# Kernel tuning notes

Hardware: AMD Instinct MI355X
Metric: run time of the kernel (lower is better)

Reference implementation:

```python
import jax, jax.numpy as jnp
import numpy as np

F, R, H = 64, 8, 128  # feature_dim, response_dim, hidden_dim
EPS = 0.1


def _mk_linear(key, fan_in, fan_out):
    kw, kb = jax.random.split(key)
    lim = 1.0 / np.sqrt(fan_in)
    W = jax.random.uniform(kw, (fan_in, fan_out), jnp.float32, -lim, lim)
    b = jax.random.uniform(kb, (fan_out,), jnp.float32, -lim, lim)
    return W, b


def setup_inputs() -> dict:
    key = jax.random.key(0)
    ks = jax.random.split(key, 8)
    n, m = 1024, 1024
    X = jax.random.normal(ks[0], (n, F), jnp.float32)
    Y = jax.random.normal(ks[1], (n, R), jnp.float32)
    U = jax.random.normal(ks[2], (m, R), jnp.float32)
    W0, b0 = _mk_linear(ks[3], F + R, H)
    W1, b1 = _mk_linear(ks[4], H, H)
    W2, b2 = _mk_linear(ks[5], H, H)
    Wout, bout = _mk_linear(ks[6], H, 1)
    return {"X": X, "Y": Y, "U": U, "W0": W0, "b0": b0, "W1": W1,
            "b1": b1, "W2": W2, "b2": b2, "Wout": Wout, "bout": bout}


def _potential(X, U, W0, b0, W1, b1, W2, b2, Wout, bout):
    # X: [n, m, F], U: [n, m, R]  -> phi: [n, m]
    z = jnp.concatenate([X, U], axis=-1)
    h = jax.nn.softplus(z @ W0 + b0)
    h = jax.nn.softplus(h @ W1 + b1)
    h = jax.nn.softplus(h @ W2 + b2)
    return (h @ Wout + bout)[..., 0]


def reference(X, Y, U, W0, b0, W1, b1, W2, b2, Wout, bout):
    n = X.shape[0]
    m = U.shape[0]
    # expand to the pairwise [n, m, .] grid (broadcast views, no copy until MLP)
    Xe = jnp.broadcast_to(X[:, None, :], (n, m, F))
    Ue = jnp.broadcast_to(U[None, :, :], (n, m, R))
    phi = _potential(Xe, Ue, W0, b0, W1, b1, W2, b2, Wout, bout)  # [n, m]
    cost = Y @ U.T                                                # [n, m]
    slack = cost - phi
    # epsilon * (logsumexp(slack/eps) - log m) == stable max-shifted form in torch source
    lme = jax.scipy.special.logsumexp(slack / EPS, axis=-1, keepdims=True)
    lme = lme - jnp.log(jnp.asarray(m, slack.dtype))
    psi = EPS * lme                                               # [n, 1]
    return psi
```

## Files before the change

### kernel.cpp

```cpp
#include <hip/hip_runtime.h>
#include <math.h>


typedef __attribute__((ext_vector_type(8))) short short8;
typedef __attribute__((ext_vector_type(4))) float f32x4;

__device__ __forceinline__ float softplus_f(float x) {
    float ax = fabsf(x);
    float t = __logf(1.0f + __expf(-ax));
    return fmaxf(x, 0.0f) + t;
}

__device__ __forceinline__ unsigned short f2bf(float x) {
    unsigned int u = __float_as_uint(x);
    u = (u + 0x7FFFu + ((u >> 16) & 1u)) >> 16;
    return (unsigned short)u;
}

__device__ __forceinline__ float bf2f(unsigned short b) {
    return __uint_as_float(((unsigned int)b) << 16);
}

__global__ __launch_bounds__(128) void prep_kernel(
    const float* __restrict__ X, const float* __restrict__ U,
    const float* __restrict__ W0, const float* __restrict__ b0,
    const float* __restrict__ W1, const float* __restrict__ W2,
    float* __restrict__ A, float* __restrict__ Bu,
    unsigned short* __restrict__ w1t, unsigned short* __restrict__ w2t)
{
    const int b = blockIdx.x, t = threadIdx.x;
    if (b < 1024) {
        const float* xr = X + b * 64;
        float s = 0.f;
        #pragma unroll 8
        for (int f = 0; f < 64; ++f) s += xr[f] * W0[f * 128 + t];
        A[b * 128 + t] = s;
    } else if (b < 2048) {
        const int j = b - 1024;
        const float* ur = U + j * 8;
        float s = b0[t];
        #pragma unroll
        for (int r = 0; r < 8; ++r) s += ur[r] * W0[(64 + r) * 128 + t];
        Bu[j * 128 + t] = s;
    } else if (b < 2176) {
        const int n = b - 2048;
        w1t[n * 128 + t] = f2bf(W1[t * 128 + n]);
    } else {
        const int n = b - 2176;
        w2t[n * 128 + t] = f2bf(W2[t * 128 + n]);
    }
}

__global__ __launch_bounds__(256, 2) void main_kernel(
    const float* __restrict__ A, const float* __restrict__ Bu,
    const unsigned short* __restrict__ w1t, const unsigned short* __restrict__ w2t,
    const float* __restrict__ Y, const float* __restrict__ U,
    const float* __restrict__ b1, const float* __restrict__ b2,
    const float* __restrict__ Wout, const float* __restrict__ bout,
    float* __restrict__ part)
{
    __shared__ __align__(16) unsigned short Ha[64][136];
    __shared__ __align__(16) unsigned short Hb[64][136];
    __shared__ __align__(16) float A_lds[16][128];
    __shared__ __align__(16) float U_lds[64][8];
    __shared__ __align__(16) float Y_lds[16][8];
    __shared__ float slk[64];

    const int tid  = threadIdx.x;
    const int lane = tid & 63;
    const int w    = tid >> 6;
    const int ib   = blockIdx.x >> 4;
    const int jb   = blockIdx.x & 15;
    const int i0   = ib * 16;
    const int j0   = jb * 64;
    const int p    = tid >> 2;
    const int q    = tid & 3;

    {
        const float4* src = (const float4*)(A + i0 * 128);
        float4* dst = (float4*)(&A_lds[0][0]);
        dst[tid] = src[tid];
        dst[tid + 256] = src[tid + 256];
        if (tid < 128) ((float4*)U_lds)[tid] = ((const float4*)(U + j0 * 8))[tid];
        else if (tid < 160) ((float4*)Y_lds)[tid - 128] = ((const float4*)(Y + i0 * 8))[tid - 128];
    }

    float bu_reg[32];
    {
        const float4* src = (const float4*)(Bu + (j0 + p) * 128 + q * 32);
        #pragma unroll
        for (int v = 0; v < 8; ++v) {
            float4 f = src[v];
            bu_reg[v * 4 + 0] = f.x; bu_reg[v * 4 + 1] = f.y;
            bu_reg[v * 4 + 2] = f.z; bu_reg[v * 4 + 3] = f.w;
        }
    }

    short8 wf[2][2][4];
    {
        const int col = lane & 15;
        const int kk  = (lane >> 4) * 8;
        #pragma unroll
        for (int nt = 0; nt < 2; ++nt)
            #pragma unroll
            for (int ks = 0; ks < 4; ++ks) {
                wf[0][nt][ks] = *(const short8*)(w1t + (w * 32 + nt * 16 + col) * 128 + ks * 32 + kk);
                wf[1][nt][ks] = *(const short8*)(w2t + (w * 32 + nt * 16 + col) * 128 + ks * 32 + kk);
            }
    }
    float rb1[2], rb2[2];
    rb1[0] = b1[w * 32 + (lane & 15)];      rb1[1] = b1[w * 32 + 16 + (lane & 15)];
    rb2[0] = b2[w * 32 + (lane & 15)];      rb2[1] = b2[w * 32 + 16 + (lane & 15)];
    const float bo = bout[0];

    __syncthreads();

    for (int rd = 0; rd < 16; ++rd) {
        {
            const float* ar = &A_lds[rd][q * 32];
            unsigned short hv[32];
            #pragma unroll
            for (int e = 0; e < 32; ++e)
                hv[e] = f2bf(softplus_f(ar[e] + bu_reg[e]));
            short8* dst = (short8*)&Ha[p][q * 32];
            #pragma unroll
            for (int v = 0; v < 4; ++v) dst[v] = ((short8*)hv)[v];
        }
        __syncthreads();

        {
            f32x4 acc[4][2];
            #pragma unroll
            for (int mt = 0; mt < 4; ++mt) {
                acc[mt][0] = (f32x4){rb1[0], rb1[0], rb1[0], rb1[0]};
                acc[mt][1] = (f32x4){rb1[1], rb1[1], rb1[1], rb1[1]};
            }
            const int col = lane & 15, kk = (lane >> 4) * 8;
            #pragma unroll
            for (int ks = 0; ks < 4; ++ks) {
                short8 a[4];
                #pragma unroll
                for (int mt = 0; mt < 4; ++mt)
                    a[mt] = *(const short8*)&Ha[mt * 16 + col][ks * 32 + kk];
                #pragma unroll
                for (int mt = 0; mt < 4; ++mt) {
                    acc[mt][0] = __builtin_amdgcn_mfma_f32_16x16x32_bf16(a[mt], wf[0][0][ks], acc[mt][0], 0, 0, 0);
                    acc[mt][1] = __builtin_amdgcn_mfma_f32_16x16x32_bf16(a[mt], wf[0][1][ks], acc[mt][1], 0, 0, 0);
                }
            }
            const int crow = (lane >> 4) * 4;
            #pragma unroll
            for (int mt = 0; mt < 4; ++mt)
                #pragma unroll
                for (int nt = 0; nt < 2; ++nt)
                    #pragma unroll
                    for (int r = 0; r < 4; ++r)
                        Hb[mt * 16 + crow + r][w * 32 + nt * 16 + col] = f2bf(softplus_f(acc[mt][nt][r]));
        }
        __syncthreads();

        {
            f32x4 acc[4][2];
            #pragma unroll
            for (int mt = 0; mt < 4; ++mt) {
                acc[mt][0] = (f32x4){rb2[0], rb2[0], rb2[0], rb2[0]};
                acc[mt][1] = (f32x4){rb2[1], rb2[1], rb2[1], rb2[1]};
            }
            const int col = lane & 15, kk = (lane >> 4) * 8;
            #pragma unroll
            for (int ks = 0; ks < 4; ++ks) {
                short8 a[4];
                #pragma unroll
                for (int mt = 0; mt < 4; ++mt)
                    a[mt] = *(const short8*)&Hb[mt * 16 + col][ks * 32 + kk];
                #pragma unroll
                for (int mt = 0; mt < 4; ++mt) {
                    acc[mt][0] = __builtin_amdgcn_mfma_f32_16x16x32_bf16(a[mt], wf[1][0][ks], acc[mt][0], 0, 0, 0);
                    acc[mt][1] = __builtin_amdgcn_mfma_f32_16x16x32_bf16(a[mt], wf[1][1][ks], acc[mt][1], 0, 0, 0);
                }
            }
            const int crow = (lane >> 4) * 4;
            #pragma unroll
            for (int mt = 0; mt < 4; ++mt)
                #pragma unroll
                for (int nt = 0; nt < 2; ++nt)
                    #pragma unroll
                    for (int r = 0; r < 4; ++r)
                        Ha[mt * 16 + crow + r][w * 32 + nt * 16 + col] = f2bf(softplus_f(acc[mt][nt][r]));
        }
        __syncthreads();

        {
            float s = 0.f;
            const float* wo = Wout + q * 32;
            const short8* hp = (const short8*)&Ha[p][q * 32];
            #pragma unroll
            for (int v = 0; v < 4; ++v) {
                short8 hh = hp[v];
                #pragma unroll
                for (int e = 0; e < 8; ++e)
                    s += bf2f((unsigned short)hh[e]) * wo[v * 8 + e];
            }
            s += __shfl_xor(s, 1);
            s += __shfl_xor(s, 2);
            if (q == 0) {
                float cost = 0.f;
                #pragma unroll
                for (int r = 0; r < 8; ++r) cost += Y_lds[rd][r] * U_lds[p][r];
                slk[p] = cost - (s + bo);
            }
        }
        __syncthreads();

        {
            float v = slk[lane];
            float m = v;
            #pragma unroll
            for (int off = 32; off; off >>= 1) m = fmaxf(m, __shfl_xor(m, off));
            float e = __expf((v - m) * 10.0f);
            #pragma unroll
            for (int off = 32; off; off >>= 1) e += __shfl_xor(e, off);
            if (tid == 0) {
                part[((i0 + rd) * 16 + jb) * 2 + 0] = m;
                part[((i0 + rd) * 16 + jb) * 2 + 1] = e;
            }
        }
        __syncthreads();
    }
}

__global__ __launch_bounds__(256) void combine_kernel(
    const float* __restrict__ part, float* __restrict__ out)
{
    const int i = blockIdx.x * 256 + threadIdx.x;
    if (i >= 1024) return;
    float M = -1e30f;
    #pragma unroll
    for (int c = 0; c < 16; ++c) M = fmaxf(M, part[(i * 16 + c) * 2 + 0]);
    float S = 0.f;
    #pragma unroll
    for (int c = 0; c < 16; ++c)
        S += part[(i * 16 + c) * 2 + 1] * __expf((part[(i * 16 + c) * 2 + 0] - M) * 10.0f);
    out[i] = M + 0.1f * (logf(S) - 6.9314718055994531f);
}

extern "C" void kernel_launch(void* const* d_in, const int* in_sizes, int n_in,
                              void* d_out, int out_size, void* d_ws, size_t ws_size,
                              hipStream_t stream) {
    const float* X    = (const float*)d_in[0];
    const float* Y    = (const float*)d_in[1];
    const float* U    = (const float*)d_in[2];
    const float* W0   = (const float*)d_in[3];
    const float* b0   = (const float*)d_in[4];
    const float* W1   = (const float*)d_in[5];
    const float* b1   = (const float*)d_in[6];
    const float* W2   = (const float*)d_in[7];
    const float* b2   = (const float*)d_in[8];
    const float* Wout = (const float*)d_in[9];
    const float* bout = (const float*)d_in[10];
    float* out = (float*)d_out;

    char* ws = (char*)d_ws;
    float*          A    = (float*)(ws);
    float*          Bu   = (float*)(ws + (512 << 10));
    unsigned short* w1t  = (unsigned short*)(ws + (1024 << 10));
    unsigned short* w2t  = (unsigned short*)(ws + (1024 << 10) + (32 << 10));
    float*          part = (float*)(ws + (1024 << 10) + (64 << 10));

    prep_kernel<<<2304, 128, 0, stream>>>(X, U, W0, b0, W1, W2, A, Bu, w1t, w2t);
    main_kernel<<<1024, 256, 0, stream>>>(A, Bu, w1t, w2t, Y, U, b1, b2, Wout, bout, part);
    combine_kernel<<<4, 256, 0, stream>>>(part, out);
}
```

Baseline: 359.5 us.

## Shrink per-block rows, drop LDS staging, pack bf16 converts, reduce per wave

Each block now processes 8 rows instead of 16, and the grid doubles. The A, U and Y LDS staging buffers are removed, so those values are read straight from global memory. Launch bounds are raised to 3 blocks per CU to lift occupancy. Float-to-bf16 rounding now uses the packed v_cvt_pk_bf16_f32 instruction, and the Wout dot product uses vector loads. The logsumexp partials are reduced per wave rather than per block, which removes one __syncthreads per row. In exchange the combine kernel reads 64 partials per row, and the higher occupancy target may cause register pressure or spills.

```diff
diff --git a/kernel.cpp b/kernel.cpp
--- a/kernel.cpp
+++ b/kernel.cpp
@@ -6,19 +6,26 @@
 typedef __attribute__((ext_vector_type(4))) float f32x4;
 
 __device__ __forceinline__ float softplus_f(float x) {
-    float ax = fabsf(x);
-    float t = __logf(1.0f + __expf(-ax));
-    return fmaxf(x, 0.0f) + t;
-}
-
-__device__ __forceinline__ unsigned short f2bf(float x) {
+    return fmaxf(x, 0.0f) + __logf(1.0f + __expf(-fabsf(x)));
+}
+
+__device__ __forceinline__ unsigned int pk_bf16(float lo, float hi) {
+    unsigned int r;
+    asm("v_cvt_pk_bf16_f32 %0, %1, %2" : "=v"(r) : "v"(lo), "v"(hi));
+    return r;
+}
+
+__device__ __forceinline__ unsigned short f2bf_prep(float x) {
     unsigned int u = __float_as_uint(x);
     u = (u + 0x7FFFu + ((u >> 16) & 1u)) >> 16;
     return (unsigned short)u;
 }
 
-__device__ __forceinline__ float bf2f(unsigned short b) {
-    return __uint_as_float(((unsigned int)b) << 16);
+__device__ __forceinline__ float bflo(unsigned int u) {
+    return __uint_as_float(u << 16);
+}
+__device__ __forceinline__ float bfhi(unsigned int u) {
+    return __uint_as_float(u & 0xFFFF0000u);
 }
 
 __global__ __launch_bounds__(128) void prep_kernel(
@@ -44,14 +51,14 @@
         Bu[j * 128 + t] = s;
     } else if (b < 2176) {
         const int n = b - 2048;
-        w1t[n * 128 + t] = f2bf(W1[t * 128 + n]);
+        w1t[n * 128 + t] = f2bf_prep(W1[t * 128 + n]);
     } else {
         const int n = b - 2176;
-        w2t[n * 128 + t] = f2bf(W2[t * 128 + n]);
-    }
-}
-
-__global__ __launch_bounds__(256, 2) void main_kernel(
+        w2t[n * 128 + t] = f2bf_prep(W2[t * 128 + n]);
+    }
+}
+
+__global__ __launch_bounds__(256, 3) void main_kernel(
     const float* __restrict__ A, const float* __restrict__ Bu,
     const unsigned short* __restrict__ w1t, const unsigned short* __restrict__ w2t,
     const float* __restrict__ Y, const float* __restrict__ U,
@@ -61,29 +68,16 @@
 {
     __shared__ __align__(16) unsigned short Ha[64][136];
     __shared__ __align__(16) unsigned short Hb[64][136];
-    __shared__ __align__(16) float A_lds[16][128];
-    __shared__ __align__(16) float U_lds[64][8];
-    __shared__ __align__(16) float Y_lds[16][8];
-    __shared__ float slk[64];
 
     const int tid  = threadIdx.x;
     const int lane = tid & 63;
     const int w    = tid >> 6;
     const int ib   = blockIdx.x >> 4;
     const int jb   = blockIdx.x & 15;
-    const int i0   = ib * 16;
+    const int i0   = ib * 8;
     const int j0   = jb * 64;
     const int p    = tid >> 2;
     const int q    = tid & 3;
-
-    {
-        const float4* src = (const float4*)(A + i0 * 128);
-        float4* dst = (float4*)(&A_lds[0][0]);
-        dst[tid] = src[tid];
-        dst[tid + 256] = src[tid + 256];
-        if (tid < 128) ((float4*)U_lds)[tid] = ((const float4*)(U + j0 * 8))[tid];
-        else if (tid < 160) ((float4*)Y_lds)[tid - 128] = ((const float4*)(Y + i0 * 8))[tid - 128];
-    }
 
     float bu_reg[32];
     {
@@ -113,20 +107,33 @@
     rb2[0] = b2[w * 32 + (lane & 15)];      rb2[1] = b2[w * 32 + 16 + (lane & 15)];
     const float bo = bout[0];
 
-    __syncthreads();
-
-    for (int rd = 0; rd < 16; ++rd) {
-        {
-            const float* ar = &A_lds[rd][q * 32];
-            unsigned short hv[32];
-            #pragma unroll
-            for (int e = 0; e < 32; ++e)
-                hv[e] = f2bf(softplus_f(ar[e] + bu_reg[e]));
-            short8* dst = (short8*)&Ha[p][q * 32];
-            #pragma unroll
-            for (int v = 0; v < 4; ++v) dst[v] = ((short8*)hv)[v];
-        }
-        __syncthreads();
+    #pragma unroll 1
+    for (int rd = 0; rd < 8; ++rd) {
+        const int i = i0 + rd;
+
+        {
+            const float4* ag = (const float4*)(A + i * 128 + q * 32);
+            unsigned int pk[16];
+            #pragma unroll
+            for (int v = 0; v < 8; ++v) {
+                float4 av = ag[v];
+                float f0 = softplus_f(av.x + bu_reg[v * 4 + 0]);
+                float f1 = softplus_f(av.y + bu_reg[v * 4 + 1]);
+                float f2 = softplus_f(av.z + bu_reg[v * 4 + 2]);
+                float f3 = softplus_f(av.w + bu_reg[v * 4 + 3]);
+                pk[v * 2 + 0] = pk_bf16(f0, f1);
+                pk[v * 2 + 1] = pk_bf16(f2, f3);
+            }
+            uint4* dst = (uint4*)&Ha[p][q * 32];
+            dst[0] = make_uint4(pk[0],  pk[1],  pk[2],  pk[3]);
+            dst[1] = make_uint4(pk[4],  pk[5],  pk[6],  pk[7]);
+            dst[2] = make_uint4(pk[8],  pk[9],  pk[10], pk[11]);
+            dst[3] = make_uint4(pk[12], pk[13], pk[14], pk[15]);
+        }
+        __syncthreads();
+
+        const int col = lane & 15, kk = (lane >> 4) * 8;
+        const int crow = (lane >> 4) * 4;
 
         {
             f32x4 acc[4][2];
@@ -135,7 +142,6 @@
                 acc[mt][0] = (f32x4){rb1[0], rb1[0], rb1[0], rb1[0]};
                 acc[mt][1] = (f32x4){rb1[1], rb1[1], rb1[1], rb1[1]};
             }
-            const int col = lane & 15, kk = (lane >> 4) * 8;
             #pragma unroll
             for (int ks = 0; ks < 4; ++ks) {
                 short8 a[4];
@@ -148,14 +154,19 @@
                     acc[mt][1] = __builtin_amdgcn_mfma_f32_16x16x32_bf16(a[mt], wf[0][1][ks], acc[mt][1], 0, 0, 0);
                 }
             }
-            const int crow = (lane >> 4) * 4;
             #pragma unroll
             for (int mt = 0; mt < 4; ++mt)
                 #pragma unroll
-                for (int nt = 0; nt < 2; ++nt)
-                    #pragma unroll
-                    for (int r = 0; r < 4; ++r)
-                        Hb[mt * 16 + crow + r][w * 32 + nt * 16 + col] = f2bf(softplus_f(acc[mt][nt][r]));
+                for (int nt = 0; nt < 2; ++nt) {
+                    unsigned int p01 = pk_bf16(softplus_f(acc[mt][nt][0]), softplus_f(acc[mt][nt][1]));
+                    unsigned int p23 = pk_bf16(softplus_f(acc[mt][nt][2]), softplus_f(acc[mt][nt][3]));
+                    const int r0 = mt * 16 + crow;
+                    const int cc = w * 32 + nt * 16 + col;
+                    Hb[r0 + 0][cc] = (unsigned short)p01;
+                    Hb[r0 + 1][cc] = (unsigned short)(p01 >> 16);
+                    Hb[r0 + 2][cc] = (unsigned short)p23;
+                    Hb[r0 + 3][cc] = (unsigned short)(p23 >> 16);
+                }
         }
         __syncthreads();
 
@@ -166,7 +177,6 @@
                 acc[mt][0] = (f32x4){rb2[0], rb2[0], rb2[0], rb2[0]};
                 acc[mt][1] = (f32x4){rb2[1], rb2[1], rb2[1], rb2[1]};
             }
-            const int col = lane & 15, kk = (lane >> 4) * 8;
             #pragma unroll
             for (int ks = 0; ks < 4; ++ks) {
                 short8 a[4];
@@ -179,50 +189,62 @@
                     acc[mt][1] = __builtin_amdgcn_mfma_f32_16x16x32_bf16(a[mt], wf[1][1][ks], acc[mt][1], 0, 0, 0);
                 }
             }
-            const int crow = (lane >> 4) * 4;
             #pragma unroll
             for (int mt = 0; mt < 4; ++mt)
                 #pragma unroll
-                for (int nt = 0; nt < 2; ++nt)
-                    #pragma unroll
-                    for (int r = 0; r < 4; ++r)
-                        Ha[mt * 16 + crow + r][w * 32 + nt * 16 + col] = f2bf(softplus_f(acc[mt][nt][r]));
-        }
-        __syncthreads();
-
-        {
+                for (int nt = 0; nt < 2; ++nt) {
+                    unsigned int p01 = pk_bf16(softplus_f(acc[mt][nt][0]), softplus_f(acc[mt][nt][1]));
+                    unsigned int p23 = pk_bf16(softplus_f(acc[mt][nt][2]), softplus_f(acc[mt][nt][3]));
+                    const int r0 = mt * 16 + crow;
+                    const int cc = w * 32 + nt * 16 + col;
+                    Ha[r0 + 0][cc] = (unsigned short)p01;
+                    Ha[r0 + 1][cc] = (unsigned short)(p01 >> 16);
+                    Ha[r0 + 2][cc] = (unsigned short)p23;
+                    Ha[r0 + 3][cc] = (unsigned short)(p23 >> 16);
+                }
+        }
+        __syncthreads();
+
+        {
+            const uint4*  hp = (const uint4*)&Ha[p][q * 32];
+            const float4* wo = (const float4*)(Wout + q * 32);
             float s = 0.f;
-            const float* wo = Wout + q * 32;
-            const short8* hp = (const short8*)&Ha[p][q * 32];
             #pragma unroll
             for (int v = 0; v < 4; ++v) {
-                short8 hh = hp[v];
-                #pragma unroll
-                for (int e = 0; e < 8; ++e)
-                    s += bf2f((unsigned short)hh[e]) * wo[v * 8 + e];
+                uint4  hh = hp[v];
+                float4 w0 = wo[v * 2 + 0];
+                float4 w1 = wo[v * 2 + 1];
+                s += bflo(hh.x) * w0.x + bfhi(hh.x) * w0.y
+                   + bflo(hh.y) * w0.z + bfhi(hh.y) * w0.w
+                   + bflo(hh.z) * w1.x + bfhi(hh.z) * w1.y
+                   + bflo(hh.w) * w1.z + bfhi(hh.w) * w1.w;
             }
             s += __shfl_xor(s, 1);
             s += __shfl_xor(s, 2);
-            if (q == 0) {
-                float cost = 0.f;
-                #pragma unroll
-                for (int r = 0; r < 8; ++r) cost += Y_lds[rd][r] * U_lds[p][r];
-                slk[p] = cost - (s + bo);
-            }
-        }
-        __syncthreads();
-
-        {
-            float v = slk[lane];
+            const float phi = s + bo;
+
+            float4 u0 = *(const float4*)(U + (j0 + p) * 8);
+            float4 u1 = *(const float4*)(U + (j0 + p) * 8 + 4);
+            float4 y0 = *(const float4*)(Y + i * 8);
+            float4 y1 = *(const float4*)(Y + i * 8 + 4);
+            float cost = u0.x * y0.x + u0.y * y0.y + u0.z * y0.z + u0.w * y0.w
+                       + u1.x * y1.x + u1.y * y1.y + u1.z * y1.z + u1.w * y1.w;
+            const float v = cost - phi;
+
             float m = v;
-            #pragma unroll
-            for (int off = 32; off; off >>= 1) m = fmaxf(m, __shfl_xor(m, off));
+            m = fmaxf(m, __shfl_xor(m, 4));
+            m = fmaxf(m, __shfl_xor(m, 8));
+            m = fmaxf(m, __shfl_xor(m, 16));
+            m = fmaxf(m, __shfl_xor(m, 32));
             float e = __expf((v - m) * 10.0f);
-            #pragma unroll
-            for (int off = 32; off; off >>= 1) e += __shfl_xor(e, off);
-            if (tid == 0) {
-                part[((i0 + rd) * 16 + jb) * 2 + 0] = m;
-                part[((i0 + rd) * 16 + jb) * 2 + 1] = e;
+            e += __shfl_xor(e, 4);
+            e += __shfl_xor(e, 8);
+            e += __shfl_xor(e, 16);
+            e += __shfl_xor(e, 32);
+            if (lane == 0) {
+                const int pi = i * 64 + jb * 4 + w;
+                part[pi * 2 + 0] = m;
+                part[pi * 2 + 1] = e * 0.25f;
             }
         }
         __syncthreads();
@@ -235,12 +257,10 @@
     const int i = blockIdx.x * 256 + threadIdx.x;
     if (i >= 1024) return;
     float M = -1e30f;
-    #pragma unroll
-    for (int c = 0; c < 16; ++c) M = fmaxf(M, part[(i * 16 + c) * 2 + 0]);
+    for (int c = 0; c < 64; ++c) M = fmaxf(M, part[(i * 64 + c) * 2 + 0]);
     float S = 0.f;
-    #pragma unroll
-    for (int c = 0; c < 16; ++c)
-        S += part[(i * 16 + c) * 2 + 1] * __expf((part[(i * 16 + c) * 2 + 0] - M) * 10.0f);
+    for (int c = 0; c < 64; ++c)
+        S += part[(i * 64 + c) * 2 + 1] * __expf((part[(i * 64 + c) * 2 + 0] - M) * 10.0f);
     out[i] = M + 0.1f * (logf(S) - 6.9314718055994531f);
 }
 
@@ -268,6 +288,6 @@
     float*          part = (float*)(ws + (1024 << 10) + (64 << 10));
 
     prep_kernel<<<2304, 128, 0, stream>>>(X, U, W0, b0, W1, W2, A, Bu, w1t, w2t);
-    main_kernel<<<1024, 256, 0, stream>>>(A, Bu, w1t, w2t, Y, U, b1, b2, Wout, bout, part);
+    main_kernel<<<2048, 256, 0, stream>>>(A, Bu, w1t, w2t, Y, U, b1, b2, Wout, bout, part);
     combine_kernel<<<4, 256, 0, stream>>>(part, out);
 }
```

After: 374.2 us. 1.04x slower.
